# Kernel optimization log

Measured on AMD Instinct MI355X. Metric: run time of the kernel, lower is better.

## Reference

```python
import jax, jax.numpy as jnp
import numpy as np

P_MASK = 0.2
HALF = (2, 25, 25)            # n_consecutive // 2 for (T, H, W)
NPIX = 5 * 51 * 51            # np.prod(n_consecutive) = 13005


def setup_inputs() -> dict:
    key = jax.random.key(0)
    ks = jax.random.split(key, 10)
    B, T, H, W, C = 4, 32, 224, 224, 3
    N = 2000
    frames = jax.random.normal(ks[0], (B, T, H, W, C), dtype=jnp.float32)
    mask_token = jax.random.normal(ks[1], (C,), dtype=jnp.float32)
    b = jax.random.randint(ks[2], (N,), 0, B)
    t = jax.random.randint(ks[3], (N,), 0, T)
    h = jax.random.randint(ks[4], (N,), 0, H)
    w = jax.random.randint(ks[5], (N,), 0, W)
    rb = jax.random.randint(ks[6], (1,), 0, B)
    rt = jax.random.randint(ks[7], (1,), 0, T)
    rh = jax.random.randint(ks[8], (1,), 0, H)
    rw = jax.random.randint(ks[9], (1,), 0, W)
    return dict(frames=frames, mask_token=mask_token, b=b, t=t, h=h, w=w,
                rb=rb, rt=rt, rh=rh, rw=rw)


def _axis_mask(idx, half, size):
    # [n_box, size] float indicator of max(0, idx-half) <= pos < min(idx+half, size-1)
    lo = jnp.maximum(idx - half, 0)[:, None]
    hi = jnp.minimum(idx + half, size - 1)[:, None]   # torch slice upper bound uses size-1
    pos = jnp.arange(size)[None, :]
    return ((pos >= lo) & (pos < hi)).astype(jnp.float32)


def _box_union(b, t, h, w, B, T, H, W):
    # union of all boxes as a single rank-1-factor contraction (no per-box scatter)
    bi = (jnp.arange(B)[None, :] == b[:, None]).astype(jnp.float32)
    ti = _axis_mask(t, HALF[0], T)
    hi = _axis_mask(h, HALF[1], H)
    wi = _axis_mask(w, HALF[2], W)
    return jnp.einsum('ib,it,ih,iw->bthw', bi, ti, hi, wi) > 0


def reference(frames, mask_token, b, t, h, w, rb, rt, rh, rw):
    B, T, H, W, C = frames.shape
    tnpix = B * T * H * W
    n1 = int(tnpix * P_MASK * 0.8 // NPIX)
    n2 = int(tnpix * P_MASK * 0.1 // NPIX)
    R1 = _box_union(b[:n1], t[:n1], h[:n1], w[:n1], B, T, H, W)
    R2 = _box_union(b[n1:n1 + n2], t[n1:n1 + n2], h[n1:n1 + n2], w[n1:n1 + n2], B, T, H, W)
    R3 = _box_union(b[n1 + n2:n1 + 2 * n2], t[n1 + n2:n1 + 2 * n2],
                    h[n1 + n2:n1 + 2 * n2], w[n1 + n2:n1 + 2 * n2], B, T, H, W)
    random_token = frames[rb[0], rt[0], rh[0], rw[0]]   # [C]
    out = jnp.where(R1[..., None], mask_token, frames)
    out = jnp.where(R2[..., None], random_token, out)
    M = (R1 | R2 | R3).reshape(B, T, -1).any(axis=-1)
    return out, M
```

## Files before the change

kernel.cpp:

```cpp
#include <hip/hip_runtime.h>

namespace {
constexpr int B_ = 4, T_ = 32, H_ = 224, W_ = 224;
constexpr int HW_ = H_ * W_;
constexpr int NPIX_ = B_ * T_ * HW_;
constexpr int N1_ = 79;
constexpr int N2_ = 9;
constexpr int NBOX_RW_ = N1_ + N2_;
constexpr int NBOX_M_  = N1_ + 2 * N2_;
constexpr int HALF_T = 2, HALF_HW = 25;
}

__global__ void build_slice_rects(
    const float* __restrict__ frames,
    const int* __restrict__ bb, const int* __restrict__ tt,
    const int* __restrict__ hh, const int* __restrict__ ww,
    const int* __restrict__ rb, const int* __restrict__ rt,
    const int* __restrict__ rh, const int* __restrict__ rw,
    int2* __restrict__ counts, int4* __restrict__ rects,
    float* __restrict__ rtok, float* __restrict__ Mout)
{
    int s = threadIdx.x;
    if (s == 0) {
        long idx = (((long)rb[0] * T_ + rt[0]) * H_ + rh[0]) * W_ + rw[0];
        rtok[0] = frames[idx * 3 + 0];
        rtok[1] = frames[idx * 3 + 1];
        rtok[2] = frames[idx * 3 + 2];
    }
    if (s >= B_ * T_) return;
    int sb = s / T_, st = s % T_;
    int c1 = 0, c2 = 0;
    bool any = false;
    for (int i = 0; i < NBOX_M_; ++i) {
        int tlo = max(tt[i] - HALF_T, 0);
        int thi = min(tt[i] + HALF_T, T_ - 1);
        if (bb[i] != sb || st < tlo || st >= thi) continue;
        any = true;
        if (i >= NBOX_RW_) continue;
        int4 r;
        r.x = max(hh[i] - HALF_HW, 0);
        r.y = min(hh[i] + HALF_HW, H_ - 1);
        r.z = max(ww[i] - HALF_HW, 0);
        r.w = min(ww[i] + HALF_HW, W_ - 1);
        if (i < N1_) rects[s * NBOX_RW_ + c1++] = r;
        else         rects[s * NBOX_RW_ + N1_ + c2++] = r;
    }
    counts[s] = make_int2(c1, c2);
    Mout[s] = any ? 1.0f : 0.0f;
}

__global__ __launch_bounds__(256) void apply_mask(
    const float* __restrict__ frames, const float* __restrict__ mtok,
    const int2* __restrict__ counts, const int4* __restrict__ rects,
    const float* __restrict__ rtok, float* __restrict__ out)
{
    int gid = blockIdx.x * blockDim.x + threadIdx.x;
    int p0 = gid * 4;
    if (p0 >= NPIX_) return;

    const float4* fin = (const float4*)(frames + (long)p0 * 3);
    float4 f0 = fin[0], f1 = fin[1], f2 = fin[2];

    int s  = p0 / HW_;
    int hw = p0 - s * HW_;
    int h  = hw / W_;
    int w0 = hw - h * W_;

    int2 c = counts[s];
    const int4* rs = rects + s * NBOX_RW_;
    int st0 = 0, st1 = 0, st2 = 0, st3 = 0;
    for (int j = 0; j < c.x; ++j) {
        int4 r = rs[j];
        if (h >= r.x && h < r.y) {
            if (w0     >= r.z && w0     < r.w) st0 = 1;
            if (w0 + 1 >= r.z && w0 + 1 < r.w) st1 = 1;
            if (w0 + 2 >= r.z && w0 + 2 < r.w) st2 = 1;
            if (w0 + 3 >= r.z && w0 + 3 < r.w) st3 = 1;
        }
    }
    for (int j = 0; j < c.y; ++j) {
        int4 r = rs[N1_ + j];
        if (h >= r.x && h < r.y) {
            if (w0     >= r.z && w0     < r.w) st0 = 2;
            if (w0 + 1 >= r.z && w0 + 1 < r.w) st1 = 2;
            if (w0 + 2 >= r.z && w0 + 2 < r.w) st2 = 2;
            if (w0 + 3 >= r.z && w0 + 3 < r.w) st3 = 2;
        }
    }

    float m0 = mtok[0], m1 = mtok[1], m2 = mtok[2];
    float r0 = rtok[0], r1 = rtok[1], r2 = rtok[2];

    float v[12] = {f0.x, f0.y, f0.z, f0.w, f1.x, f1.y, f1.z, f1.w,
                   f2.x, f2.y, f2.z, f2.w};
    int stk[4] = {st0, st1, st2, st3};
#pragma unroll
    for (int k = 0; k < 4; ++k) {
        int state = stk[k];
        v[k * 3 + 0] = (state == 2) ? r0 : ((state == 1) ? m0 : v[k * 3 + 0]);
        v[k * 3 + 1] = (state == 2) ? r1 : ((state == 1) ? m1 : v[k * 3 + 1]);
        v[k * 3 + 2] = (state == 2) ? r2 : ((state == 1) ? m2 : v[k * 3 + 2]);
    }

    float4* fo = (float4*)(out + (long)p0 * 3);
    fo[0] = make_float4(v[0], v[1], v[2], v[3]);
    fo[1] = make_float4(v[4], v[5], v[6], v[7]);
    fo[2] = make_float4(v[8], v[9], v[10], v[11]);
}

extern "C" void kernel_launch(void* const* d_in, const int* in_sizes, int n_in,
                              void* d_out, int out_size, void* d_ws, size_t ws_size,
                              hipStream_t stream)
{
    const float* frames = (const float*)d_in[0];
    const float* mtok   = (const float*)d_in[1];
    const int* b  = (const int*)d_in[2];
    const int* t  = (const int*)d_in[3];
    const int* h  = (const int*)d_in[4];
    const int* w  = (const int*)d_in[5];
    const int* rb = (const int*)d_in[6];
    const int* rt = (const int*)d_in[7];
    const int* rh = (const int*)d_in[8];
    const int* rw = (const int*)d_in[9];

    int2*  counts = (int2*)d_ws;
    int4*  rects  = (int4*)((char*)d_ws + 1024);
    float* rtok   = (float*)((char*)d_ws + 1024 + (size_t)128 * NBOX_RW_ * 16);

    float* out_frames = (float*)d_out;
    float* out_M      = out_frames + (long)NPIX_ * 3;

    build_slice_rects<<<1, 128, 0, stream>>>(frames, b, t, h, w, rb, rt, rh, rw,
                                             counts, rects, rtok, out_M);

    int nthreads = NPIX_ / 4;
    apply_mask<<<nthreads / 256, 256, 0, stream>>>(frames, mtok, counts, rects,
                                                   rtok, out_frames);
}
```

Before: 174.6 us.

## Process eight pixels per thread with bitmask box tests and shared box staging

The apply kernel now handles eight pixels (six float4 loads and stores) per thread, halving the per-pixel cost of the rectangle scan. Per-pixel comparisons are replaced by a bitmask built from each box's clipped w range, and the select step is skipped when no pixel is covered. The setup kernel stages the box parameters in shared memory once instead of every thread re-reading and re-deriving them from global memory. The grid halves, which may reduce latency hiding for what is mostly a bandwidth-bound copy.

```diff
diff --git a/kernel.cpp b/kernel.cpp
--- a/kernel.cpp
+++ b/kernel.cpp
@@ -11,7 +11,7 @@
 constexpr int HALF_T = 2, HALF_HW = 25;
 }
 
-__global__ void build_slice_rects(
+__global__ __launch_bounds__(128) void build_slice_rects(
     const float* __restrict__ frames,
     const int* __restrict__ bb, const int* __restrict__ tt,
     const int* __restrict__ hh, const int* __restrict__ ww,
@@ -20,6 +20,9 @@
     int2* __restrict__ counts, int4* __restrict__ rects,
     float* __restrict__ rtok, float* __restrict__ Mout)
 {
+    __shared__ int lb[NBOX_M_], ltlo[NBOX_M_], lthi[NBOX_M_];
+    __shared__ int4 lrect[NBOX_M_];
+
     int s = threadIdx.x;
     if (s == 0) {
         long idx = (((long)rb[0] * T_ + rt[0]) * H_ + rh[0]) * W_ + rw[0];
@@ -27,23 +30,29 @@
         rtok[1] = frames[idx * 3 + 1];
         rtok[2] = frames[idx * 3 + 2];
     }
-    if (s >= B_ * T_) return;
+    if (s < NBOX_M_) {
+        lb[s]   = bb[s];
+        ltlo[s] = max(tt[s] - HALF_T, 0);
+        lthi[s] = min(tt[s] + HALF_T, T_ - 1);
+        int4 r;
+        r.x = max(hh[s] - HALF_HW, 0);
+        r.y = min(hh[s] + HALF_HW, H_ - 1);
+        r.z = max(ww[s] - HALF_HW, 0);
+        r.w = min(ww[s] + HALF_HW, W_ - 1);
+        lrect[s] = r;
+    }
+    __syncthreads();
+
     int sb = s / T_, st = s % T_;
     int c1 = 0, c2 = 0;
     bool any = false;
+    int4* rs = rects + s * NBOX_RW_;
     for (int i = 0; i < NBOX_M_; ++i) {
-        int tlo = max(tt[i] - HALF_T, 0);
-        int thi = min(tt[i] + HALF_T, T_ - 1);
-        if (bb[i] != sb || st < tlo || st >= thi) continue;
+        if (lb[i] != sb || st < ltlo[i] || st >= lthi[i]) continue;
         any = true;
         if (i >= NBOX_RW_) continue;
-        int4 r;
-        r.x = max(hh[i] - HALF_HW, 0);
-        r.y = min(hh[i] + HALF_HW, H_ - 1);
-        r.z = max(ww[i] - HALF_HW, 0);
-        r.w = min(ww[i] + HALF_HW, W_ - 1);
-        if (i < N1_) rects[s * NBOX_RW_ + c1++] = r;
-        else         rects[s * NBOX_RW_ + N1_ + c2++] = r;
+        if (i < N1_) rs[c1++] = lrect[i];
+        else         rs[N1_ + c2++] = lrect[i];
     }
     counts[s] = make_int2(c1, c2);
     Mout[s] = any ? 1.0f : 0.0f;
@@ -55,11 +64,12 @@
     const float* __restrict__ rtok, float* __restrict__ out)
 {
     int gid = blockIdx.x * blockDim.x + threadIdx.x;
-    int p0 = gid * 4;
-    if (p0 >= NPIX_) return;
+    int p0 = gid * 8;
 
     const float4* fin = (const float4*)(frames + (long)p0 * 3);
-    float4 f0 = fin[0], f1 = fin[1], f2 = fin[2];
+    float4 f[6];
+#pragma unroll
+    for (int k = 0; k < 6; ++k) f[k] = fin[k];
 
     int s  = p0 / HW_;
     int hw = p0 - s * HW_;
@@ -68,44 +78,38 @@
 
     int2 c = counts[s];
     const int4* rs = rects + s * NBOX_RW_;
-    int st0 = 0, st1 = 0, st2 = 0, st3 = 0;
+    unsigned m1 = 0, m2 = 0;
     for (int j = 0; j < c.x; ++j) {
         int4 r = rs[j];
         if (h >= r.x && h < r.y) {
-            if (w0     >= r.z && w0     < r.w) st0 = 1;
-            if (w0 + 1 >= r.z && w0 + 1 < r.w) st1 = 1;
-            if (w0 + 2 >= r.z && w0 + 2 < r.w) st2 = 1;
-            if (w0 + 3 >= r.z && w0 + 3 < r.w) st3 = 1;
+            int lo = max(r.z - w0, 0), hi = min(r.w - w0, 8);
+            if (hi > lo) m1 |= ((1u << (hi - lo)) - 1u) << lo;
         }
     }
     for (int j = 0; j < c.y; ++j) {
         int4 r = rs[N1_ + j];
         if (h >= r.x && h < r.y) {
-            if (w0     >= r.z && w0     < r.w) st0 = 2;
-            if (w0 + 1 >= r.z && w0 + 1 < r.w) st1 = 2;
-            if (w0 + 2 >= r.z && w0 + 2 < r.w) st2 = 2;
-            if (w0 + 3 >= r.z && w0 + 3 < r.w) st3 = 2;
+            int lo = max(r.z - w0, 0), hi = min(r.w - w0, 8);
+            if (hi > lo) m2 |= ((1u << (hi - lo)) - 1u) << lo;
         }
     }
 
-    float m0 = mtok[0], m1 = mtok[1], m2 = mtok[2];
-    float r0 = rtok[0], r1 = rtok[1], r2 = rtok[2];
-
-    float v[12] = {f0.x, f0.y, f0.z, f0.w, f1.x, f1.y, f1.z, f1.w,
-                   f2.x, f2.y, f2.z, f2.w};
-    int stk[4] = {st0, st1, st2, st3};
+    if (m1 | m2) {
+        float mt0 = mtok[0], mt1 = mtok[1], mt2 = mtok[2];
+        float rt0 = rtok[0], rt1 = rtok[1], rt2 = rtok[2];
+        float* v = (float*)f;
 #pragma unroll
-    for (int k = 0; k < 4; ++k) {
-        int state = stk[k];
-        v[k * 3 + 0] = (state == 2) ? r0 : ((state == 1) ? m0 : v[k * 3 + 0]);
-        v[k * 3 + 1] = (state == 2) ? r1 : ((state == 1) ? m1 : v[k * 3 + 1]);
-        v[k * 3 + 2] = (state == 2) ? r2 : ((state == 1) ? m2 : v[k * 3 + 2]);
+        for (int k = 0; k < 8; ++k) {
+            bool b2 = (m2 >> k) & 1u, b1 = (m1 >> k) & 1u;
+            v[k * 3 + 0] = b2 ? rt0 : (b1 ? mt0 : v[k * 3 + 0]);
+            v[k * 3 + 1] = b2 ? rt1 : (b1 ? mt1 : v[k * 3 + 1]);
+            v[k * 3 + 2] = b2 ? rt2 : (b1 ? mt2 : v[k * 3 + 2]);
+        }
     }
 
     float4* fo = (float4*)(out + (long)p0 * 3);
-    fo[0] = make_float4(v[0], v[1], v[2], v[3]);
-    fo[1] = make_float4(v[4], v[5], v[6], v[7]);
-    fo[2] = make_float4(v[8], v[9], v[10], v[11]);
+#pragma unroll
+    for (int k = 0; k < 6; ++k) fo[k] = f[k];
 }
 
 extern "C" void kernel_launch(void* const* d_in, const int* in_sizes, int n_in,
@@ -133,7 +137,7 @@
     build_slice_rects<<<1, 128, 0, stream>>>(frames, b, t, h, w, rb, rt, rh, rw,
                                              counts, rects, rtok, out_M);
 
-    int nthreads = NPIX_ / 4;
+    int nthreads = NPIX_ / 8;
     apply_mask<<<nthreads / 256, 256, 0, stream>>>(frames, mtok, counts, rects,
                                                    rtok, out_frames);
 }
```

Result: no change. 176.4 us (+1.0%).
